# Kernel optimization log

Hardware: AMD Instinct MI355X
Metric: run time of the kernel (lower is better)

The kernel has to match this reference:

```python
import jax, jax.numpy as jnp
import numpy as np

SR = 2  # sr_ratio

def _avgpool2x2(x):
    # x: [B,C,H,W] -> [B,C,H//2,W//2]
    B, C, H, W = x.shape
    return x.reshape(B, C, H // SR, SR, W // SR, SR).mean(axis=(3, 5))

def setup_inputs() -> dict:
    key = jax.random.key(0)
    ks = jax.random.split(key, 6)
    B, C, H, W = 8, 256, 64, 64
    d = C // 8
    sc_qk = 1.0 / np.sqrt(C)
    return {
        "x": jax.random.normal(ks[0], (B, C, H, W), jnp.float32),
        "wq": jax.random.normal(ks[1], (d, C), jnp.float32) * sc_qk,
        "wk": jax.random.normal(ks[2], (d, C), jnp.float32) * sc_qk,
        "wv": jax.random.normal(ks[3], (C, C), jnp.float32) * sc_qk,
        "wo": jax.random.normal(ks[4], (C, C), jnp.float32) * sc_qk,
        "gamma": jax.random.normal(ks[5], (1,), jnp.float32),
    }

def reference(x, wq, wk, wv, wo, gamma):
    B, C, H, W = x.shape
    N = H * W
    d = wq.shape[0]
    # q: conv1x1 then flatten+transpose -> [B, N, d]
    q = jnp.einsum('dc,bchw->bhwd', wq, x).reshape(B, N, d)
    # spatial reduction of K/V source
    x_kv = _avgpool2x2(x)
    Hk, Wk = x_kv.shape[2], x_kv.shape[3]
    Nk = Hk * Wk
    k = jnp.einsum('dc,bchw->bdhw', wk, x_kv).reshape(B, d, Nk)   # [B,d,Nk]
    v = jnp.einsum('oc,bchw->bohw', wv, x_kv).reshape(B, C, Nk)   # [B,C,Nk]
    # attn = softmax(q @ k / sqrt(d)) over Nk
    attn = jax.nn.softmax(jnp.einsum('bnd,bdm->bnm', q, k) / jnp.sqrt(jnp.float32(d)), axis=-1)
    # out = v @ attn^T -> [B,C,N]
    out = jnp.einsum('bcm,bnm->bcn', v, attn).reshape(B, C, H, W)
    out = jnp.einsum('oc,bchw->bohw', wo, out)
    return x + gamma[0] * out
```

## Files before the change

### kernel.cpp

```cpp
#include <hip/hip_runtime.h>

#define BB 8
#define CC 256
#define NN 4096
#define DD 32
#define NK 1024

typedef unsigned short u16;
typedef unsigned int   u32;
typedef __attribute__((ext_vector_type(8))) short bf16x8;
typedef __attribute__((ext_vector_type(4))) float f32x4;

#define MFMA16 __builtin_amdgcn_mfma_f32_16x16x32_bf16

#define OFF_WVO  0u
#define OFF_WQB  32768u
#define OFF_WKB  36864u
#define OFF_QF   40960u
#define OFF_KF   565248u
#define OFF_VOF  696320u

__device__ __forceinline__ u16 f2bf(float f) {
    u32 u = __float_as_uint(f);
    u += 0x7FFFu + ((u >> 16) & 1u);
    return (u16)(u >> 16);
}

__device__ __forceinline__ u32 cvt_pk_bf16(float lo, float hi) {
    u32 r;
    asm("v_cvt_pk_bf16_f32 %0, %1, %2" : "=v"(r) : "v"(lo), "v"(hi));
    return r;
}

__launch_bounds__(1024)
__global__ void wprep_kernel(const float* __restrict__ wq, const float* __restrict__ wk,
                             const float* __restrict__ wv, const float* __restrict__ wo,
                             u16* __restrict__ wqb, u16* __restrict__ wkb,
                             u16* __restrict__ wvob) {
    __shared__ float part[4][256];
    int o = blockIdx.x, t = threadIdx.x;
    int jq = t >> 8, c = t & 255;
    const float* wvp = wv + (size_t)(jq * 64) * CC + c;
    const float* wop = wo + o * CC + jq * 64;
    float acc = 0.f;
#pragma unroll 8
    for (int i = 0; i < 64; ++i)
        acc += wop[i] * wvp[(size_t)i * CC];
    part[jq][c] = acc;
    __syncthreads();
    if (t < 256)
        wvob[o * CC + t] = f2bf(part[0][t] + part[1][t] + part[2][t] + part[3][t]);
    if (o < 8) {
        const float QS = 0.17677669529663687f * 1.4426950408889634f;
        int id = o * 1024 + t;
        wqb[id] = f2bf(wq[id] * QS);
    } else if (o < 16) {
        int id = (o - 8) * 1024 + t;
        wkb[id] = f2bf(wk[id]);
    }
}

__launch_bounds__(256)
__global__ void proj_kernel(const float* __restrict__ x,
                            const u16* __restrict__ wqb, const u16* __restrict__ wkb,
                            const u16* __restrict__ wvob,
                            u16* __restrict__ qF, u16* __restrict__ kF,
                            u16* __restrict__ voF) {
    int t = threadIdx.x, w = t >> 6, l = t & 63, l15 = l & 15, lg = l >> 4;
    const f32x4 fz = {0.f, 0.f, 0.f, 0.f};

    if (blockIdx.x < 256) {
        __shared__ float xl[64 * 136];
        int b = blockIdx.x & 7, nb = blockIdx.x >> 3;
        int n0 = nb * 128;
        f32x4 acc[2][2];
        acc[0][0] = fz; acc[0][1] = fz; acc[1][0] = fz; acc[1][1] = fz;
        int cr = t >> 2, seg = (t & 3) * 32;
        for (int ch = 0; ch < 4; ++ch) {
            int c0 = ch * 64;
            const float* xs = x + ((size_t)(b * CC + c0 + cr)) * NN + n0 + seg;
#pragma unroll
            for (int p = 0; p < 8; ++p)
                *(float4*)&xl[cr * 136 + seg + p * 4] = *(const float4*)(xs + p * 4);
            __syncthreads();
#pragma unroll
            for (int ks = 0; ks < 2; ++ks) {
                int klo = ks * 32 + lg * 8;
#pragma unroll
                for (int i = 0; i < 2; ++i) {
                    int nl = w * 32 + i * 16 + l15;
                    float f0 = xl[(klo + 0) * 136 + nl];
                    float f1 = xl[(klo + 1) * 136 + nl];
                    float f2 = xl[(klo + 2) * 136 + nl];
                    float f3 = xl[(klo + 3) * 136 + nl];
                    float f4 = xl[(klo + 4) * 136 + nl];
                    float f5 = xl[(klo + 5) * 136 + nl];
                    float f6 = xl[(klo + 6) * 136 + nl];
                    float f7 = xl[(klo + 7) * 136 + nl];
                    union { u32 u[4]; bf16x8 v; } cv;
                    cv.u[0] = cvt_pk_bf16(f0, f1);
                    cv.u[1] = cvt_pk_bf16(f2, f3);
                    cv.u[2] = cvt_pk_bf16(f4, f5);
                    cv.u[3] = cvt_pk_bf16(f6, f7);
#pragma unroll
                    for (int dt = 0; dt < 2; ++dt) {
                        bf16x8 bq = *(const bf16x8*)(wqb + (size_t)(dt * 16 + l15) * CC + c0 + klo);
                        acc[i][dt] = MFMA16(cv.v, bq, acc[i][dt], 0, 0, 0);
                    }
                }
            }
            __syncthreads();
        }
        u16* outp = qF + (size_t)b * 256 * 512;
#pragma unroll
        for (int i = 0; i < 2; ++i)
#pragma unroll
            for (int dt = 0; dt < 2; ++dt)
#pragma unroll
                for (int r2 = 0; r2 < 4; ++r2) {
                    int tile = nb * 8 + w * 2 + i;
                    int dhi = dt * 2 + (l15 >> 3);
                    outp[((size_t)tile * 64 + dhi * 16 + lg * 4 + r2) * 8 + (l15 & 7)]
                        = f2bf(acc[i][dt][r2]);
                }
    } else {
        __shared__ u16 pl[64 * 42];
        int blk2 = blockIdx.x - 256;
        int b = blk2 & 7, hk = blk2 >> 3;
        f32x4 acck = fz;
        f32x4 accv[2][4];
#pragma unroll
        for (int mt = 0; mt < 2; ++mt)
#pragma unroll
            for (int ot = 0; ot < 4; ++ot) accv[mt][ot] = fz;

        int cr = t >> 2, w8 = (t & 3) * 8;
        for (int ch = 0; ch < 4; ++ch) {
            int c0 = ch * 64;
            const float* xs = x + ((size_t)(b * CC + c0 + cr)) * NN + (2 * hk) * 64 + w8 * 2;
            float4 A0 = *(const float4*)(xs +  0), A1 = *(const float4*)(xs +  4);
            float4 A2 = *(const float4*)(xs +  8), A3 = *(const float4*)(xs + 12);
            float4 B0 = *(const float4*)(xs + 64), B1 = *(const float4*)(xs + 68);
            float4 B2 = *(const float4*)(xs + 72), B3 = *(const float4*)(xs + 76);
            float p0 = 0.25f * (A0.x + A0.y + B0.x + B0.y);
            float p1 = 0.25f * (A0.z + A0.w + B0.z + B0.w);
            float p2 = 0.25f * (A1.x + A1.y + B1.x + B1.y);
            float p3 = 0.25f * (A1.z + A1.w + B1.z + B1.w);
            float p4 = 0.25f * (A2.x + A2.y + B2.x + B2.y);
            float p5 = 0.25f * (A2.z + A2.w + B2.z + B2.w);
            float p6 = 0.25f * (A3.x + A3.y + B3.x + B3.y);
            float p7 = 0.25f * (A3.z + A3.w + B3.z + B3.w);
            u32* pw = (u32*)&pl[cr * 42 + w8];
            pw[0] = cvt_pk_bf16(p0, p1);
            pw[1] = cvt_pk_bf16(p2, p3);
            pw[2] = cvt_pk_bf16(p4, p5);
            pw[3] = cvt_pk_bf16(p6, p7);
            __syncthreads();
#pragma unroll
            for (int ks = 0; ks < 2; ++ks) {
                int klo = ks * 32 + lg * 8;
                bf16x8 pm[2];
#pragma unroll
                for (int mt = 0; mt < 2; ++mt) {
                    union { u16 s[8]; bf16x8 v; } cv;
#pragma unroll
                    for (int j = 0; j < 8; ++j)
                        cv.s[j] = pl[(klo + j) * 42 + mt * 16 + l15];
                    pm[mt] = cv.v;
                }
                {
                    bf16x8 bk = *(const bf16x8*)(wkb + (size_t)((w & 1) * 16 + l15) * CC + c0 + klo);
                    acck = MFMA16(pm[w >> 1], bk, acck, 0, 0, 0);
                }
#pragma unroll
                for (int ot = 0; ot < 4; ++ot) {
                    bf16x8 ao = *(const bf16x8*)(wvob + (size_t)(w * 64 + ot * 16 + l15) * CC + c0 + klo);
#pragma unroll
                    for (int mt = 0; mt < 2; ++mt)
                        accv[mt][ot] = MFMA16(ao, pm[mt], accv[mt][ot], 0, 0, 0);
                }
            }
            __syncthreads();
        }
#pragma unroll
        for (int r2 = 0; r2 < 4; ++r2)
            kF[((size_t)(b * 64 + hk * 2 + (w >> 1)) * 64
                + ((w & 1) * 2 + (l15 >> 3)) * 16 + lg * 4 + r2) * 8 + (l15 & 7)]
                = f2bf(acck[r2]);
#pragma unroll
        for (int mt = 0; mt < 2; ++mt)
#pragma unroll
            for (int ot = 0; ot < 4; ++ot)
#pragma unroll
                for (int r2 = 0; r2 < 4; ++r2)
                    voF[(((size_t)(b * 32 + hk) * 16 + w * 4 + ot) * 64
                         + (mt * 2 + (l15 >> 3)) * 16 + lg * 4 + r2) * 8 + (l15 & 7)]
                        = f2bf(accv[mt][ot][r2]);
    }
}

__launch_bounds__(512, 4)
__global__ void attn_kernel(const u16* __restrict__ qF, const u16* __restrict__ kF,
                            const u16* __restrict__ voF, const float* __restrict__ x,
                            const float* __restrict__ gamma, float* __restrict__ out) {
    __shared__ __align__(16) u16   p_lds[2][2][64 * 40];
    __shared__ __align__(16) float rs_lds[2][64];

    const int t   = threadIdx.x;
    const int wv  = t >> 6, l = t & 63;
    const int wm  = wv >> 2, wo = wv & 3;
    const int l15 = l & 15, lg = l >> 4;
    const int b   = blockIdx.x & 7;
    const int n0  = (blockIdx.x >> 3) << 6;

    bf16x8 qf = *(const bf16x8*)(qF + ((size_t)(b * 256 + (n0 >> 4) + wo) * 64 + l) * 8);
    const u16* kfp = kF  + ((size_t)(b * 64 + wm * 32) * 64 + l) * 8;
    const u16* vbl = voF + ((size_t)((b * 32 + wm * 16) * 16 + wo * 4) * 64 + l) * 8;

    u16*       pwp = &p_lds[wm][0][(wo * 16 + l15) * 40 + lg * 4];
    const u16* prp = &p_lds[wm][0][l15 * 40 + lg * 8];

    f32x4 acc[4][4];
    const f32x4 fz = {0.f, 0.f, 0.f, 0.f};
#pragma unroll
    for (int j = 0; j < 4; ++j)
#pragma unroll
        for (int of = 0; of < 4; ++of) acc[j][of] = fz;
    float rs = 0.f;

    bf16x8 kf0 = *(const bf16x8*)(kfp);
    bf16x8 kf1 = *(const bf16x8*)(kfp + 512);

#pragma unroll 2
    for (int i = 0; i < 16; ++i) {
        const int buf = i & 1;
        bf16x8 vof[4];
#pragma unroll
        for (int of = 0; of < 4; ++of)
            vof[of] = *(const bf16x8*)(vbl + (size_t)i * 8192 + of * 512);
        f32x4 c0 = MFMA16(kf0, qf, fz, 0, 0, 0);
        f32x4 c1 = MFMA16(kf1, qf, fz, 0, 0, 0);
        float e0 = __builtin_amdgcn_exp2f(c0[0]);
        float e1 = __builtin_amdgcn_exp2f(c0[1]);
        float e2 = __builtin_amdgcn_exp2f(c0[2]);
        float e3 = __builtin_amdgcn_exp2f(c0[3]);
        float e4 = __builtin_amdgcn_exp2f(c1[0]);
        float e5 = __builtin_amdgcn_exp2f(c1[1]);
        float e6 = __builtin_amdgcn_exp2f(c1[2]);
        float e7 = __builtin_amdgcn_exp2f(c1[3]);
        rs += (e0 + e1 + e2 + e3) + (e4 + e5 + e6 + e7);
        uint2 pw0, pw1;
        pw0.x = cvt_pk_bf16(e0, e1);
        pw0.y = cvt_pk_bf16(e2, e3);
        pw1.x = cvt_pk_bf16(e4, e5);
        pw1.y = cvt_pk_bf16(e6, e7);
        u16* pw = pwp + buf * 2560;
        *(uint2*)pw        = pw0;
        *(uint2*)(pw + 16) = pw1;
        asm volatile("s_waitcnt lgkmcnt(0)" ::: "memory");
        __builtin_amdgcn_s_barrier();
        bf16x8 kn0, kn1;
        if (i < 15) {
            kn0 = *(const bf16x8*)(kfp + (size_t)(i * 2 + 2) * 512);
            kn1 = *(const bf16x8*)(kfp + (size_t)(i * 2 + 3) * 512);
        }
        const u16* pr = prp + buf * 2560;
        __builtin_amdgcn_s_setprio(1);
#pragma unroll
        for (int j = 0; j < 4; ++j) {
            bf16x8 pa = *(const bf16x8*)(pr + j * 640);
#pragma unroll
            for (int of = 0; of < 4; ++of)
                acc[j][of] = MFMA16(pa, vof[of], acc[j][of], 0, 0, 0);
        }
        __builtin_amdgcn_s_setprio(0);
        kf0 = kn0; kf1 = kn1;
    }

    rs += __shfl_xor(rs, 16);
    rs += __shfl_xor(rs, 32);
    if (l < 16) rs_lds[wm][wo * 16 + l] = rs;

    __syncthreads();
    float* cbuf = (float*)p_lds;
#pragma unroll
    for (int r = 0; r < 4; ++r) {
        if (wm == 1) {
#pragma unroll
            for (int of = 0; of < 4; ++of)
                *(float4*)&cbuf[((wo * 64 + l) * 16) + of * 4] =
                    make_float4(acc[r][of][0], acc[r][of][1], acc[r][of][2], acc[r][of][3]);
        }
        __syncthreads();
        if (wm == 0) {
#pragma unroll
            for (int of = 0; of < 4; ++of) {
                float4 p = *(const float4*)&cbuf[((wo * 64 + l) * 16) + of * 4];
                acc[r][of][0] += p.x; acc[r][of][1] += p.y;
                acc[r][of][2] += p.z; acc[r][of][3] += p.w;
            }
        }
        __syncthreads();
    }

    if (wm == 0) {
        float g = gamma[0];
#pragma unroll
        for (int j = 0; j < 4; ++j) {
            float r0 = rs_lds[0][j * 16 + lg * 4 + 0] + rs_lds[1][j * 16 + lg * 4 + 0];
            float r1 = rs_lds[0][j * 16 + lg * 4 + 1] + rs_lds[1][j * 16 + lg * 4 + 1];
            float r2 = rs_lds[0][j * 16 + lg * 4 + 2] + rs_lds[1][j * 16 + lg * 4 + 2];
            float r3 = rs_lds[0][j * 16 + lg * 4 + 3] + rs_lds[1][j * 16 + lg * 4 + 3];
            float fa0 = g / r0, fa1 = g / r1, fa2 = g / r2, fa3 = g / r3;
#pragma unroll
            for (int of = 0; of < 4; ++of) {
                size_t base = ((size_t)(b * CC + wo * 64 + of * 16 + l15)) * NN
                            + n0 + j * 16 + lg * 4;
                float4 xv = *(const float4*)(x + base);
                float4 ov;
                ov.x = xv.x + acc[j][of][0] * fa0;
                ov.y = xv.y + acc[j][of][1] * fa1;
                ov.z = xv.z + acc[j][of][2] * fa2;
                ov.w = xv.w + acc[j][of][3] * fa3;
                *(float4*)(out + base) = ov;
            }
        }
    }
}

extern "C" void kernel_launch(void* const* d_in, const int* in_sizes, int n_in,
                              void* d_out, int out_size, void* d_ws, size_t ws_size,
                              hipStream_t stream) {
    const float* x     = (const float*)d_in[0];
    const float* wq    = (const float*)d_in[1];
    const float* wk    = (const float*)d_in[2];
    const float* wv    = (const float*)d_in[3];
    const float* wo    = (const float*)d_in[4];
    const float* gamma = (const float*)d_in[5];
    float* out = (float*)d_out;
    float* ws  = (float*)d_ws;

    u16* wvob = (u16*)(ws + OFF_WVO);
    u16* wqb  = (u16*)(ws + OFF_WQB);
    u16* wkb  = (u16*)(ws + OFF_WKB);
    u16* qF   = (u16*)(ws + OFF_QF);
    u16* kF   = (u16*)(ws + OFF_KF);
    u16* voF  = (u16*)(ws + OFF_VOF);

    wprep_kernel<<<dim3(256), dim3(1024), 0, stream>>>(wq, wk, wv, wo, wqb, wkb, wvob);
    proj_kernel <<<dim3(512), dim3(256),  0, stream>>>(x, wqb, wkb, wvob, qF, kF, voF);
    attn_kernel <<<dim3(512), dim3(512),  0, stream>>>(qF, kF, voF, x, gamma, out);
}
```

Baseline: 59.59 us.

## Fuse Q and KV projection blocks and restructure attention split over query rows

The projection kernel now has each block load an x tile once and produce both the Q projection and the pooled K/V projections from the same shared-memory tile. It also prefetches the next channel chunk into registers. This halves the x global reads and the grid size. The attention kernel now splits waves over query rows instead of over the key dimension, which removes the cross-wave LDS reduction of accumulators. It also software-pipelines the QK exp step one iteration ahead of the PV MFMAs. In exchange there are fewer blocks (256), lower occupancy (launch bounds 2), and a longer serial loop per wave.

```diff
diff --git a/kernel.cpp b/kernel.cpp
--- a/kernel.cpp
+++ b/kernel.cpp
@@ -66,51 +66,108 @@
                             const u16* __restrict__ wvob,
                             u16* __restrict__ qF, u16* __restrict__ kF,
                             u16* __restrict__ voF) {
+    __shared__ float xl[64 * 136];
+    __shared__ u16 pl[64 * 42];
     int t = threadIdx.x, w = t >> 6, l = t & 63, l15 = l & 15, lg = l >> 4;
     const f32x4 fz = {0.f, 0.f, 0.f, 0.f};
-
-    if (blockIdx.x < 256) {
-        __shared__ float xl[64 * 136];
-        int b = blockIdx.x & 7, nb = blockIdx.x >> 3;
-        int n0 = nb * 128;
-        f32x4 acc[2][2];
-        acc[0][0] = fz; acc[0][1] = fz; acc[1][0] = fz; acc[1][1] = fz;
-        int cr = t >> 2, seg = (t & 3) * 32;
-        for (int ch = 0; ch < 4; ++ch) {
-            int c0 = ch * 64;
-            const float* xs = x + ((size_t)(b * CC + c0 + cr)) * NN + n0 + seg;
-#pragma unroll
-            for (int p = 0; p < 8; ++p)
-                *(float4*)&xl[cr * 136 + seg + p * 4] = *(const float4*)(xs + p * 4);
-            __syncthreads();
-#pragma unroll
-            for (int ks = 0; ks < 2; ++ks) {
-                int klo = ks * 32 + lg * 8;
-#pragma unroll
-                for (int i = 0; i < 2; ++i) {
-                    int nl = w * 32 + i * 16 + l15;
-                    float f0 = xl[(klo + 0) * 136 + nl];
-                    float f1 = xl[(klo + 1) * 136 + nl];
-                    float f2 = xl[(klo + 2) * 136 + nl];
-                    float f3 = xl[(klo + 3) * 136 + nl];
-                    float f4 = xl[(klo + 4) * 136 + nl];
-                    float f5 = xl[(klo + 5) * 136 + nl];
-                    float f6 = xl[(klo + 6) * 136 + nl];
-                    float f7 = xl[(klo + 7) * 136 + nl];
-                    union { u32 u[4]; bf16x8 v; } cv;
-                    cv.u[0] = cvt_pk_bf16(f0, f1);
-                    cv.u[1] = cvt_pk_bf16(f2, f3);
-                    cv.u[2] = cvt_pk_bf16(f4, f5);
-                    cv.u[3] = cvt_pk_bf16(f6, f7);
-#pragma unroll
-                    for (int dt = 0; dt < 2; ++dt) {
-                        bf16x8 bq = *(const bf16x8*)(wqb + (size_t)(dt * 16 + l15) * CC + c0 + klo);
-                        acc[i][dt] = MFMA16(cv.v, bq, acc[i][dt], 0, 0, 0);
-                    }
+    int b = blockIdx.x & 7, hb = blockIdx.x >> 3;
+    int n0 = hb * 128;
+
+    int cr = t >> 2, seg = (t & 3) * 32, w8 = (t & 3) * 8;
+
+    f32x4 qacc[2][2];
+    qacc[0][0] = fz; qacc[0][1] = fz; qacc[1][0] = fz; qacc[1][1] = fz;
+    f32x4 kacc = fz;
+    f32x4 vacc[2][4];
+#pragma unroll
+    for (int mt = 0; mt < 2; ++mt)
+#pragma unroll
+        for (int ot = 0; ot < 4; ++ot) vacc[mt][ot] = fz;
+
+    float4 xreg[8];
+    {
+        const float* xs = x + ((size_t)(b * CC + cr)) * NN + n0 + seg;
+#pragma unroll
+        for (int p = 0; p < 8; ++p) xreg[p] = *(const float4*)(xs + p * 4);
+    }
+
+    for (int ch = 0; ch < 4; ++ch) {
+        int c0 = ch * 64;
+#pragma unroll
+        for (int p = 0; p < 8; ++p)
+            *(float4*)&xl[cr * 136 + seg + p * 4] = xreg[p];
+        __syncthreads();
+        if (ch < 3) {
+            const float* xs = x + ((size_t)(b * CC + c0 + 64 + cr)) * NN + n0 + seg;
+#pragma unroll
+            for (int p = 0; p < 8; ++p) xreg[p] = *(const float4*)(xs + p * 4);
+        }
+        {
+            const float* xr = &xl[cr * 136];
+            u32 pw[4];
+#pragma unroll
+            for (int j = 0; j < 4; ++j) {
+                int q0 = 2 * (w8 + 2 * j), q1 = 2 * (w8 + 2 * j + 1);
+                float v0 = 0.25f * (xr[q0] + xr[q0 + 1] + xr[64 + q0] + xr[65 + q0]);
+                float v1 = 0.25f * (xr[q1] + xr[q1 + 1] + xr[64 + q1] + xr[65 + q1]);
+                pw[j] = cvt_pk_bf16(v0, v1);
+            }
+            u32* pd = (u32*)&pl[cr * 42 + w8];
+            pd[0] = pw[0]; pd[1] = pw[1]; pd[2] = pw[2]; pd[3] = pw[3];
+        }
+#pragma unroll
+        for (int ks = 0; ks < 2; ++ks) {
+            int klo = ks * 32 + lg * 8;
+#pragma unroll
+            for (int i = 0; i < 2; ++i) {
+                int nl = w * 32 + i * 16 + l15;
+                float f0 = xl[(klo + 0) * 136 + nl];
+                float f1 = xl[(klo + 1) * 136 + nl];
+                float f2 = xl[(klo + 2) * 136 + nl];
+                float f3 = xl[(klo + 3) * 136 + nl];
+                float f4 = xl[(klo + 4) * 136 + nl];
+                float f5 = xl[(klo + 5) * 136 + nl];
+                float f6 = xl[(klo + 6) * 136 + nl];
+                float f7 = xl[(klo + 7) * 136 + nl];
+                union { u32 u[4]; bf16x8 v; } cv;
+                cv.u[0] = cvt_pk_bf16(f0, f1);
+                cv.u[1] = cvt_pk_bf16(f2, f3);
+                cv.u[2] = cvt_pk_bf16(f4, f5);
+                cv.u[3] = cvt_pk_bf16(f6, f7);
+#pragma unroll
+                for (int dt = 0; dt < 2; ++dt) {
+                    bf16x8 bq = *(const bf16x8*)(wqb + (size_t)(dt * 16 + l15) * CC + c0 + klo);
+                    qacc[i][dt] = MFMA16(cv.v, bq, qacc[i][dt], 0, 0, 0);
                 }
             }
-            __syncthreads();
-        }
+        }
+        __syncthreads();
+#pragma unroll
+        for (int ks = 0; ks < 2; ++ks) {
+            int klo = ks * 32 + lg * 8;
+            bf16x8 pm[2];
+#pragma unroll
+            for (int mt = 0; mt < 2; ++mt) {
+                union { u16 s[8]; bf16x8 v; } cv;
+#pragma unroll
+                for (int j = 0; j < 8; ++j)
+                    cv.s[j] = pl[(klo + j) * 42 + mt * 16 + l15];
+                pm[mt] = cv.v;
+            }
+            {
+                bf16x8 bk = *(const bf16x8*)(wkb + (size_t)((w & 1) * 16 + l15) * CC + c0 + klo);
+                kacc = MFMA16(pm[w >> 1], bk, kacc, 0, 0, 0);
+            }
+#pragma unroll
+            for (int ot = 0; ot < 4; ++ot) {
+                bf16x8 ao = *(const bf16x8*)(wvob + (size_t)(w * 64 + ot * 16 + l15) * CC + c0 + klo);
+#pragma unroll
+                for (int mt = 0; mt < 2; ++mt)
+                    vacc[mt][ot] = MFMA16(ao, pm[mt], vacc[mt][ot], 0, 0, 0);
+            }
+        }
+    }
+    {
         u16* outp = qF + (size_t)b * 256 * 512;
 #pragma unroll
         for (int i = 0; i < 2; ++i)
@@ -118,107 +175,48 @@
             for (int dt = 0; dt < 2; ++dt)
 #pragma unroll
                 for (int r2 = 0; r2 < 4; ++r2) {
-                    int tile = nb * 8 + w * 2 + i;
+                    int tile = hb * 8 + w * 2 + i;
                     int dhi = dt * 2 + (l15 >> 3);
                     outp[((size_t)tile * 64 + dhi * 16 + lg * 4 + r2) * 8 + (l15 & 7)]
-                        = f2bf(acc[i][dt][r2]);
+                        = f2bf(qacc[i][dt][r2]);
                 }
-    } else {
-        __shared__ u16 pl[64 * 42];
-        int blk2 = blockIdx.x - 256;
-        int b = blk2 & 7, hk = blk2 >> 3;
-        f32x4 acck = fz;
-        f32x4 accv[2][4];
-#pragma unroll
-        for (int mt = 0; mt < 2; ++mt)
-#pragma unroll
-            for (int ot = 0; ot < 4; ++ot) accv[mt][ot] = fz;
-
-        int cr = t >> 2, w8 = (t & 3) * 8;
-        for (int ch = 0; ch < 4; ++ch) {
-            int c0 = ch * 64;
-            const float* xs = x + ((size_t)(b * CC + c0 + cr)) * NN + (2 * hk) * 64 + w8 * 2;
-            float4 A0 = *(const float4*)(xs +  0), A1 = *(const float4*)(xs +  4);
-            float4 A2 = *(const float4*)(xs +  8), A3 = *(const float4*)(xs + 12);
-            float4 B0 = *(const float4*)(xs + 64), B1 = *(const float4*)(xs + 68);
-            float4 B2 = *(const float4*)(xs + 72), B3 = *(const float4*)(xs + 76);
-            float p0 = 0.25f * (A0.x + A0.y + B0.x + B0.y);
-            float p1 = 0.25f * (A0.z + A0.w + B0.z + B0.w);
-            float p2 = 0.25f * (A1.x + A1.y + B1.x + B1.y);
-            float p3 = 0.25f * (A1.z + A1.w + B1.z + B1.w);
-            float p4 = 0.25f * (A2.x + A2.y + B2.x + B2.y);
-            float p5 = 0.25f * (A2.z + A2.w + B2.z + B2.w);
-            float p6 = 0.25f * (A3.x + A3.y + B3.x + B3.y);
-            float p7 = 0.25f * (A3.z + A3.w + B3.z + B3.w);
-            u32* pw = (u32*)&pl[cr * 42 + w8];
-            pw[0] = cvt_pk_bf16(p0, p1);
-            pw[1] = cvt_pk_bf16(p2, p3);
-            pw[2] = cvt_pk_bf16(p4, p5);
-            pw[3] = cvt_pk_bf16(p6, p7);
-            __syncthreads();
-#pragma unroll
-            for (int ks = 0; ks < 2; ++ks) {
-                int klo = ks * 32 + lg * 8;
-                bf16x8 pm[2];
-#pragma unroll
-                for (int mt = 0; mt < 2; ++mt) {
-                    union { u16 s[8]; bf16x8 v; } cv;
-#pragma unroll
-                    for (int j = 0; j < 8; ++j)
-                        cv.s[j] = pl[(klo + j) * 42 + mt * 16 + l15];
-                    pm[mt] = cv.v;
-                }
-                {
-                    bf16x8 bk = *(const bf16x8*)(wkb + (size_t)((w & 1) * 16 + l15) * CC + c0 + klo);
-                    acck = MFMA16(pm[w >> 1], bk, acck, 0, 0, 0);
-                }
-#pragma unroll
-                for (int ot = 0; ot < 4; ++ot) {
-                    bf16x8 ao = *(const bf16x8*)(wvob + (size_t)(w * 64 + ot * 16 + l15) * CC + c0 + klo);
-#pragma unroll
-                    for (int mt = 0; mt < 2; ++mt)
-                        accv[mt][ot] = MFMA16(ao, pm[mt], accv[mt][ot], 0, 0, 0);
-                }
-            }
-            __syncthreads();
-        }
-#pragma unroll
-        for (int r2 = 0; r2 < 4; ++r2)
-            kF[((size_t)(b * 64 + hk * 2 + (w >> 1)) * 64
-                + ((w & 1) * 2 + (l15 >> 3)) * 16 + lg * 4 + r2) * 8 + (l15 & 7)]
-                = f2bf(acck[r2]);
-#pragma unroll
-        for (int mt = 0; mt < 2; ++mt)
-#pragma unroll
-            for (int ot = 0; ot < 4; ++ot)
-#pragma unroll
-                for (int r2 = 0; r2 < 4; ++r2)
-                    voF[(((size_t)(b * 32 + hk) * 16 + w * 4 + ot) * 64
-                         + (mt * 2 + (l15 >> 3)) * 16 + lg * 4 + r2) * 8 + (l15 & 7)]
-                        = f2bf(accv[mt][ot][r2]);
-    }
-}
-
-__launch_bounds__(512, 4)
+    }
+#pragma unroll
+    for (int r2 = 0; r2 < 4; ++r2)
+        kF[((size_t)(b * 64 + hb * 2 + (w >> 1)) * 64
+            + ((w & 1) * 2 + (l15 >> 3)) * 16 + lg * 4 + r2) * 8 + (l15 & 7)]
+            = f2bf(kacc[r2]);
+#pragma unroll
+    for (int mt = 0; mt < 2; ++mt)
+#pragma unroll
+        for (int ot = 0; ot < 4; ++ot)
+#pragma unroll
+            for (int r2 = 0; r2 < 4; ++r2)
+                voF[(((size_t)(b * 32 + hb) * 16 + w * 4 + ot) * 64
+                     + (mt * 2 + (l15 >> 3)) * 16 + lg * 4 + r2) * 8 + (l15 & 7)]
+                    = f2bf(vacc[mt][ot][r2]);
+}
+
+__launch_bounds__(512, 2)
 __global__ void attn_kernel(const u16* __restrict__ qF, const u16* __restrict__ kF,
                             const u16* __restrict__ voF, const float* __restrict__ x,
                             const float* __restrict__ gamma, float* __restrict__ out) {
     __shared__ __align__(16) u16   p_lds[2][2][64 * 40];
-    __shared__ __align__(16) float rs_lds[2][64];
+    __shared__ __align__(16) float rs_lds[128];
 
     const int t   = threadIdx.x;
     const int wv  = t >> 6, l = t & 63;
-    const int wm  = wv >> 2, wo = wv & 3;
+    const int nh  = wv >> 2, wo4 = wv & 3;
     const int l15 = l & 15, lg = l >> 4;
     const int b   = blockIdx.x & 7;
-    const int n0  = (blockIdx.x >> 3) << 6;
-
-    bf16x8 qf = *(const bf16x8*)(qF + ((size_t)(b * 256 + (n0 >> 4) + wo) * 64 + l) * 8);
-    const u16* kfp = kF  + ((size_t)(b * 64 + wm * 32) * 64 + l) * 8;
-    const u16* vbl = voF + ((size_t)((b * 32 + wm * 16) * 16 + wo * 4) * 64 + l) * 8;
-
-    u16*       pwp = &p_lds[wm][0][(wo * 16 + l15) * 40 + lg * 4];
-    const u16* prp = &p_lds[wm][0][l15 * 40 + lg * 8];
+    const int n0  = (blockIdx.x >> 3) << 7;
+
+    bf16x8 qf = *(const bf16x8*)(qF + ((size_t)(b * 256 + (n0 >> 4) + nh * 4 + wo4) * 64 + l) * 8);
+    const u16* kfp = kF  + ((size_t)(b * 64) * 64 + l) * 8;
+    const u16* vbl = voF + ((size_t)((b * 32) * 16 + wo4 * 4) * 64 + l) * 8;
+
+    u16*       pwp = &p_lds[nh][0][(wo4 * 16 + l15) * 40 + lg * 4];
+    const u16* prp = &p_lds[nh][0][l15 * 40 + lg * 8];
 
     f32x4 acc[4][4];
     const f32x4 fz = {0.f, 0.f, 0.f, 0.f};
@@ -230,14 +228,7 @@
 
     bf16x8 kf0 = *(const bf16x8*)(kfp);
     bf16x8 kf1 = *(const bf16x8*)(kfp + 512);
-
-#pragma unroll 2
-    for (int i = 0; i < 16; ++i) {
-        const int buf = i & 1;
-        bf16x8 vof[4];
-#pragma unroll
-        for (int of = 0; of < 4; ++of)
-            vof[of] = *(const bf16x8*)(vbl + (size_t)i * 8192 + of * 512);
+    {
         f32x4 c0 = MFMA16(kf0, qf, fz, 0, 0, 0);
         f32x4 c1 = MFMA16(kf1, qf, fz, 0, 0, 0);
         float e0 = __builtin_amdgcn_exp2f(c0[0]);
@@ -254,76 +245,86 @@
         pw0.y = cvt_pk_bf16(e2, e3);
         pw1.x = cvt_pk_bf16(e4, e5);
         pw1.y = cvt_pk_bf16(e6, e7);
-        u16* pw = pwp + buf * 2560;
-        *(uint2*)pw        = pw0;
-        *(uint2*)(pw + 16) = pw1;
+        *(uint2*)pwp        = pw0;
+        *(uint2*)(pwp + 16) = pw1;
+    }
+    kf0 = *(const bf16x8*)(kfp + 2 * 512);
+    kf1 = *(const bf16x8*)(kfp + 3 * 512);
+    asm volatile("s_waitcnt lgkmcnt(0)" ::: "memory");
+    __builtin_amdgcn_s_barrier();
+
+#pragma unroll 2
+    for (int i = 0; i < 32; ++i) {
+        const int buf = i & 1;
+        bf16x8 vof[4];
+#pragma unroll
+        for (int of = 0; of < 4; ++of)
+            vof[of] = *(const bf16x8*)(vbl + (size_t)i * 8192 + of * 512);
+        bf16x8 kn0, kn1;
+        if (i < 31) {
+            f32x4 c0 = MFMA16(kf0, qf, fz, 0, 0, 0);
+            f32x4 c1 = MFMA16(kf1, qf, fz, 0, 0, 0);
+            if (i < 30) {
+                kn0 = *(const bf16x8*)(kfp + (size_t)(2 * i + 4) * 512);
+                kn1 = *(const bf16x8*)(kfp + (size_t)(2 * i + 5) * 512);
+            }
+            float e0 = __builtin_amdgcn_exp2f(c0[0]);
+            float e1 = __builtin_amdgcn_exp2f(c0[1]);
+            float e2 = __builtin_amdgcn_exp2f(c0[2]);
+            float e3 = __builtin_amdgcn_exp2f(c0[3]);
+            float e4 = __builtin_amdgcn_exp2f(c1[0]);
+            float e5 = __builtin_amdgcn_exp2f(c1[1]);
+            float e6 = __builtin_amdgcn_exp2f(c1[2]);
+            float e7 = __builtin_amdgcn_exp2f(c1[3]);
+            rs += (e0 + e1 + e2 + e3) + (e4 + e5 + e6 + e7);
+            uint2 pw0, pw1;
+            pw0.x = cvt_pk_bf16(e0, e1);
+            pw0.y = cvt_pk_bf16(e2, e3);
+            pw1.x = cvt_pk_bf16(e4, e5);
+            pw1.y = cvt_pk_bf16(e6, e7);
+            u16* pw = pwp + (buf ^ 1) * 2560;
+            *(uint2*)pw        = pw0;
+            *(uint2*)(pw + 16) = pw1;
+        }
+        const u16* pr = prp + buf * 2560;
+        __builtin_amdgcn_s_setprio(1);
+#pragma unroll
+        for (int j = 0; j < 4; ++j) {
+            bf16x8 pa = *(const bf16x8*)(pr + j * 640);
+#pragma unroll
+            for (int of = 0; of < 4; ++of)
+                acc[j][of] = MFMA16(pa, vof[of], acc[j][of], 0, 0, 0);
+        }
+        __builtin_amdgcn_s_setprio(0);
         asm volatile("s_waitcnt lgkmcnt(0)" ::: "memory");
         __builtin_amdgcn_s_barrier();
-        bf16x8 kn0, kn1;
-        if (i < 15) {
-            kn0 = *(const bf16x8*)(kfp + (size_t)(i * 2 + 2) * 512);
-            kn1 = *(const bf16x8*)(kfp + (size_t)(i * 2 + 3) * 512);
-        }
-        const u16* pr = prp + buf * 2560;
-        __builtin_amdgcn_s_setprio(1);
-#pragma unroll
-        for (int j = 0; j < 4; ++j) {
-            bf16x8 pa = *(const bf16x8*)(pr + j * 640);
-#pragma unroll
-            for (int of = 0; of < 4; ++of)
-                acc[j][of] = MFMA16(pa, vof[of], acc[j][of], 0, 0, 0);
-        }
-        __builtin_amdgcn_s_setprio(0);
         kf0 = kn0; kf1 = kn1;
     }
 
     rs += __shfl_xor(rs, 16);
     rs += __shfl_xor(rs, 32);
-    if (l < 16) rs_lds[wm][wo * 16 + l] = rs;
-
+    if (l < 16) rs_lds[nh * 64 + wo4 * 16 + l] = rs;
     __syncthreads();
-    float* cbuf = (float*)p_lds;
-#pragma unroll
-    for (int r = 0; r < 4; ++r) {
-        if (wm == 1) {
-#pragma unroll
-            for (int of = 0; of < 4; ++of)
-                *(float4*)&cbuf[((wo * 64 + l) * 16) + of * 4] =
-                    make_float4(acc[r][of][0], acc[r][of][1], acc[r][of][2], acc[r][of][3]);
-        }
-        __syncthreads();
-        if (wm == 0) {
-#pragma unroll
-            for (int of = 0; of < 4; ++of) {
-                float4 p = *(const float4*)&cbuf[((wo * 64 + l) * 16) + of * 4];
-                acc[r][of][0] += p.x; acc[r][of][1] += p.y;
-                acc[r][of][2] += p.z; acc[r][of][3] += p.w;
-            }
-        }
-        __syncthreads();
-    }
-
-    if (wm == 0) {
-        float g = gamma[0];
-#pragma unroll
-        for (int j = 0; j < 4; ++j) {
-            float r0 = rs_lds[0][j * 16 + lg * 4 + 0] + rs_lds[1][j * 16 + lg * 4 + 0];
-            float r1 = rs_lds[0][j * 16 + lg * 4 + 1] + rs_lds[1][j * 16 + lg * 4 + 1];
-            float r2 = rs_lds[0][j * 16 + lg * 4 + 2] + rs_lds[1][j * 16 + lg * 4 + 2];
-            float r3 = rs_lds[0][j * 16 + lg * 4 + 3] + rs_lds[1][j * 16 + lg * 4 + 3];
-            float fa0 = g / r0, fa1 = g / r1, fa2 = g / r2, fa3 = g / r3;
-#pragma unroll
-            for (int of = 0; of < 4; ++of) {
-                size_t base = ((size_t)(b * CC + wo * 64 + of * 16 + l15)) * NN
-                            + n0 + j * 16 + lg * 4;
-                float4 xv = *(const float4*)(x + base);
-                float4 ov;
-                ov.x = xv.x + acc[j][of][0] * fa0;
-                ov.y = xv.y + acc[j][of][1] * fa1;
-                ov.z = xv.z + acc[j][of][2] * fa2;
-                ov.w = xv.w + acc[j][of][3] * fa3;
-                *(float4*)(out + base) = ov;
-            }
+
+    float g = gamma[0];
+#pragma unroll
+    for (int j = 0; j < 4; ++j) {
+        int rbase = nh * 64 + j * 16 + lg * 4;
+        float fa0 = g / rs_lds[rbase + 0];
+        float fa1 = g / rs_lds[rbase + 1];
+        float fa2 = g / rs_lds[rbase + 2];
+        float fa3 = g / rs_lds[rbase + 3];
+#pragma unroll
+        for (int of = 0; of < 4; ++of) {
+            size_t base = ((size_t)(b * CC + wo4 * 64 + of * 16 + l15)) * NN
+                        + n0 + nh * 64 + j * 16 + lg * 4;
+            float4 xv = *(const float4*)(x + base);
+            float4 ov;
+            ov.x = xv.x + acc[j][of][0] * fa0;
+            ov.y = xv.y + acc[j][of][1] * fa1;
+            ov.z = xv.z + acc[j][of][2] * fa2;
+            ov.w = xv.w + acc[j][of][3] * fa3;
+            *(float4*)(out + base) = ov;
         }
     }
 }
@@ -348,6 +349,6 @@
     u16* voF  = (u16*)(ws + OFF_VOF);
 
     wprep_kernel<<<dim3(256), dim3(1024), 0, stream>>>(wq, wk, wv, wo, wqb, wkb, wvob);
-    proj_kernel <<<dim3(512), dim3(256),  0, stream>>>(x, wqb, wkb, wvob, qF, kF, voF);
-    attn_kernel <<<dim3(512), dim3(512),  0, stream>>>(qF, kF, voF, x, gamma, out);
-}
+    proj_kernel <<<dim3(256), dim3(256),  0, stream>>>(x, wqb, wkb, wvob, qF, kF, voF);
+    attn_kernel <<<dim3(256), dim3(512),  0, stream>>>(qF, kF, voF, x, gamma, out);
+}
```

New measurement: 71.93 us. 20.7% more time.

## Software-pipeline QK^T/exp stage one tile ahead of PV MFMAs

Applied to the files above, without the earlier changes.

Peels the first score tile (QK MFMA, exp2, bf16 pack, LDS store) into a prologue. Inside the loop it computes the next tile's probabilities into the other LDS buffer while doing the PV MFMAs on the current buffer. The result is one barrier per iteration placed after both stages, so exp/MFMA latency of the next tile overlaps the current accumulation. This costs extra register pressure and more complex control flow at the loop tail.

```diff
diff --git a/kernel.cpp b/kernel.cpp
--- a/kernel.cpp
+++ b/kernel.cpp
@@ -230,14 +230,7 @@
 
     bf16x8 kf0 = *(const bf16x8*)(kfp);
     bf16x8 kf1 = *(const bf16x8*)(kfp + 512);
-
-#pragma unroll 2
-    for (int i = 0; i < 16; ++i) {
-        const int buf = i & 1;
-        bf16x8 vof[4];
-#pragma unroll
-        for (int of = 0; of < 4; ++of)
-            vof[of] = *(const bf16x8*)(vbl + (size_t)i * 8192 + of * 512);
+    {
         f32x4 c0 = MFMA16(kf0, qf, fz, 0, 0, 0);
         f32x4 c1 = MFMA16(kf1, qf, fz, 0, 0, 0);
         float e0 = __builtin_amdgcn_exp2f(c0[0]);
@@ -254,26 +247,59 @@
         pw0.y = cvt_pk_bf16(e2, e3);
         pw1.x = cvt_pk_bf16(e4, e5);
         pw1.y = cvt_pk_bf16(e6, e7);
-        u16* pw = pwp + buf * 2560;
-        *(uint2*)pw        = pw0;
-        *(uint2*)(pw + 16) = pw1;
+        *(uint2*)pwp        = pw0;
+        *(uint2*)(pwp + 16) = pw1;
+    }
+    kf0 = *(const bf16x8*)(kfp + 2 * 512);
+    kf1 = *(const bf16x8*)(kfp + 3 * 512);
+    asm volatile("s_waitcnt lgkmcnt(0)" ::: "memory");
+    __builtin_amdgcn_s_barrier();
+
+#pragma unroll 2
+    for (int i = 0; i < 16; ++i) {
+        const int buf = i & 1;
+        bf16x8 vof[4];
+#pragma unroll
+        for (int of = 0; of < 4; ++of)
+            vof[of] = *(const bf16x8*)(vbl + (size_t)i * 8192 + of * 512);
+        bf16x8 kn0, kn1;
+        if (i < 15) {
+            f32x4 c0 = MFMA16(kf0, qf, fz, 0, 0, 0);
+            f32x4 c1 = MFMA16(kf1, qf, fz, 0, 0, 0);
+            if (i < 14) {
+                kn0 = *(const bf16x8*)(kfp + (size_t)(2 * i + 4) * 512);
+                kn1 = *(const bf16x8*)(kfp + (size_t)(2 * i + 5) * 512);
+            }
+            float e0 = __builtin_amdgcn_exp2f(c0[0]);
+            float e1 = __builtin_amdgcn_exp2f(c0[1]);
+            float e2 = __builtin_amdgcn_exp2f(c0[2]);
+            float e3 = __builtin_amdgcn_exp2f(c0[3]);
+            float e4 = __builtin_amdgcn_exp2f(c1[0]);
+            float e5 = __builtin_amdgcn_exp2f(c1[1]);
+            float e6 = __builtin_amdgcn_exp2f(c1[2]);
+            float e7 = __builtin_amdgcn_exp2f(c1[3]);
+            rs += (e0 + e1 + e2 + e3) + (e4 + e5 + e6 + e7);
+            uint2 pw0, pw1;
+            pw0.x = cvt_pk_bf16(e0, e1);
+            pw0.y = cvt_pk_bf16(e2, e3);
+            pw1.x = cvt_pk_bf16(e4, e5);
+            pw1.y = cvt_pk_bf16(e6, e7);
+            u16* pw = pwp + (buf ^ 1) * 2560;
+            *(uint2*)pw        = pw0;
+            *(uint2*)(pw + 16) = pw1;
+        }
+        const u16* pr = prp + buf * 2560;
+        __builtin_amdgcn_s_setprio(1);
+#pragma unroll
+        for (int j = 0; j < 4; ++j) {
+            bf16x8 pa = *(const bf16x8*)(pr + j * 640);
+#pragma unroll
+            for (int of = 0; of < 4; ++of)
+                acc[j][of] = MFMA16(pa, vof[of], acc[j][of], 0, 0, 0);
+        }
+        __builtin_amdgcn_s_setprio(0);
         asm volatile("s_waitcnt lgkmcnt(0)" ::: "memory");
         __builtin_amdgcn_s_barrier();
-        bf16x8 kn0, kn1;
-        if (i < 15) {
-            kn0 = *(const bf16x8*)(kfp + (size_t)(i * 2 + 2) * 512);
-            kn1 = *(const bf16x8*)(kfp + (size_t)(i * 2 + 3) * 512);
-        }
-        const u16* pr = prp + buf * 2560;
-        __builtin_amdgcn_s_setprio(1);
-#pragma unroll
-        for (int j = 0; j < 4; ++j) {
-            bf16x8 pa = *(const bf16x8*)(pr + j * 640);
-#pragma unroll
-            for (int of = 0; of < 4; ++of)
-                acc[j][of] = MFMA16(pa, vof[of], acc[j][of], 0, 0, 0);
-        }
-        __builtin_amdgcn_s_setprio(0);
         kf0 = kn0; kf1 = kn1;
     }
 
```

Result: no change. 59.88 us (+0.5%).

## Switch attention kernel to 32x32 MFMA with register-shuffled probabilities

Applied to the files above, without the earlier changes.

Rewrites the attention kernel to use 32x32x16 bf16 MFMA tiles, so each wave computes a full 32-query score block and feeds the exponentiated probabilities straight back as the A operand via cross-half lane shuffles instead of staging them through LDS with barriers. Work is split by query chunk and output-channel half, and each wave loops over all 1024 keys, which removes the cross-wave LDS reduction of partial outputs. The proj kernel's Q/K/VO output layouts are changed to match the 32x32 fragment format. The trade-off is fewer threads per block, more accumulator registers per wave, and each wave re-reading K and VO for the whole key range.

```diff
diff --git a/kernel.cpp b/kernel.cpp
--- a/kernel.cpp
+++ b/kernel.cpp
@@ -8,10 +8,12 @@
 
 typedef unsigned short u16;
 typedef unsigned int   u32;
-typedef __attribute__((ext_vector_type(8))) short bf16x8;
-typedef __attribute__((ext_vector_type(4))) float f32x4;
+typedef __attribute__((ext_vector_type(8)))  short bf16x8;
+typedef __attribute__((ext_vector_type(4)))  float f32x4;
+typedef __attribute__((ext_vector_type(16))) float f32x16;
 
 #define MFMA16 __builtin_amdgcn_mfma_f32_16x16x32_bf16
+#define MFMA32 __builtin_amdgcn_mfma_f32_32x32x16_bf16
 
 #define OFF_WVO  0u
 #define OFF_WQB  32768u
@@ -111,17 +113,16 @@
             }
             __syncthreads();
         }
-        u16* outp = qF + (size_t)b * 256 * 512;
+        u16* outp = qF + (size_t)b * 131072;
 #pragma unroll
         for (int i = 0; i < 2; ++i)
 #pragma unroll
             for (int dt = 0; dt < 2; ++dt)
 #pragma unroll
                 for (int r2 = 0; r2 < 4; ++r2) {
-                    int tile = nb * 8 + w * 2 + i;
-                    int dhi = dt * 2 + (l15 >> 3);
-                    outp[((size_t)tile * 64 + dhi * 16 + lg * 4 + r2) * 8 + (l15 & 7)]
-                        = f2bf(acc[i][dt][r2]);
+                    int n = nb * 128 + w * 32 + i * 16 + lg * 4 + r2;
+                    outp[(((size_t)(n >> 5) * 2 + dt) * 64 + (n & 31) + 32 * (l15 >> 3)) * 8
+                         + (l15 & 7)] = f2bf(acc[i][dt][r2]);
                 }
     } else {
         __shared__ u16 pl[64 * 42];
@@ -183,147 +184,123 @@
             __syncthreads();
         }
 #pragma unroll
-        for (int r2 = 0; r2 < 4; ++r2)
-            kF[((size_t)(b * 64 + hk * 2 + (w >> 1)) * 64
-                + ((w & 1) * 2 + (l15 >> 3)) * 16 + lg * 4 + r2) * 8 + (l15 & 7)]
+        for (int r2 = 0; r2 < 4; ++r2) {
+            int m31 = (w >> 1) * 16 + lg * 4 + r2;
+            kF[(size_t)b * 32768
+               + (((size_t)hk * 2 + (w & 1)) * 64 + m31 + 32 * (l15 >> 3)) * 8 + (l15 & 7)]
                 = f2bf(acck[r2]);
+        }
 #pragma unroll
         for (int mt = 0; mt < 2; ++mt)
 #pragma unroll
             for (int ot = 0; ot < 4; ++ot)
 #pragma unroll
-                for (int r2 = 0; r2 < 4; ++r2)
-                    voF[(((size_t)(b * 32 + hk) * 16 + w * 4 + ot) * 64
-                         + (mt * 2 + (l15 >> 3)) * 16 + lg * 4 + r2) * 8 + (l15 & 7)]
-                        = f2bf(accv[mt][ot][r2]);
+                for (int r2 = 0; r2 < 4; ++r2) {
+                    int o  = w * 64 + ot * 16 + lg * 4 + r2;
+                    int m16c = hk * 2 + mt;
+                    voF[(size_t)b * 262144
+                        + (((size_t)m16c * 8 + (o >> 5)) * 64 + (o & 31) + 32 * (l15 >> 3)) * 8
+                        + (l15 & 7)] = f2bf(accv[mt][ot][r2]);
+                }
     }
 }
 
-__launch_bounds__(512, 4)
+__launch_bounds__(256, 2)
 __global__ void attn_kernel(const u16* __restrict__ qF, const u16* __restrict__ kF,
                             const u16* __restrict__ voF, const float* __restrict__ x,
                             const float* __restrict__ gamma, float* __restrict__ out) {
-    __shared__ __align__(16) u16   p_lds[2][2][64 * 40];
-    __shared__ __align__(16) float rs_lds[2][64];
+    __shared__ float rs_lds[4][32];
 
     const int t   = threadIdx.x;
-    const int wv  = t >> 6, l = t & 63;
-    const int wm  = wv >> 2, wo = wv & 3;
-    const int l15 = l & 15, lg = l >> 4;
+    const int w   = t >> 6, l = t & 63;
+    const int l31 = l & 31, hi = l >> 5;
     const int b   = blockIdx.x & 7;
-    const int n0  = (blockIdx.x >> 3) << 6;
-
-    bf16x8 qf = *(const bf16x8*)(qF + ((size_t)(b * 256 + (n0 >> 4) + wo) * 64 + l) * 8);
-    const u16* kfp = kF  + ((size_t)(b * 64 + wm * 32) * 64 + l) * 8;
-    const u16* vbl = voF + ((size_t)((b * 32 + wm * 16) * 16 + wo * 4) * 64 + l) * 8;
-
-    u16*       pwp = &p_lds[wm][0][(wo * 16 + l15) * 40 + lg * 4];
-    const u16* prp = &p_lds[wm][0][l15 * 40 + lg * 8];
-
-    f32x4 acc[4][4];
-    const f32x4 fz = {0.f, 0.f, 0.f, 0.f};
-#pragma unroll
-    for (int j = 0; j < 4; ++j)
-#pragma unroll
-        for (int of = 0; of < 4; ++of) acc[j][of] = fz;
+    const int rem = blockIdx.x >> 3;
+    const int oh  = rem & 1;
+    const int nc  = (rem >> 1) * 4 + w;
+
+    const u16* qb = qF  + (size_t)b * 131072;
+    const u16* kb = kF  + (size_t)b * 32768;
+    const u16* vb = voF + (size_t)b * 262144;
+
+    bf16x8 qf0 = *(const bf16x8*)(qb + ((size_t)(nc * 2 + 0) * 64 + l) * 8);
+    bf16x8 qf1 = *(const bf16x8*)(qb + ((size_t)(nc * 2 + 1) * 64 + l) * 8);
+
+    f32x16 acc[4];
+    f32x16 fz16;
+#pragma unroll
+    for (int i = 0; i < 16; ++i) fz16[i] = 0.f;
+#pragma unroll
+    for (int c = 0; c < 4; ++c) acc[c] = fz16;
     float rs = 0.f;
 
-    bf16x8 kf0 = *(const bf16x8*)(kfp);
-    bf16x8 kf1 = *(const bf16x8*)(kfp + 512);
-
-#pragma unroll 2
-    for (int i = 0; i < 16; ++i) {
-        const int buf = i & 1;
-        bf16x8 vof[4];
-#pragma unroll
-        for (int of = 0; of < 4; ++of)
-            vof[of] = *(const bf16x8*)(vbl + (size_t)i * 8192 + of * 512);
-        f32x4 c0 = MFMA16(kf0, qf, fz, 0, 0, 0);
-        f32x4 c1 = MFMA16(kf1, qf, fz, 0, 0, 0);
-        float e0 = __builtin_amdgcn_exp2f(c0[0]);
-        float e1 = __builtin_amdgcn_exp2f(c0[1]);
-        float e2 = __builtin_amdgcn_exp2f(c0[2]);
-        float e3 = __builtin_amdgcn_exp2f(c0[3]);
-        float e4 = __builtin_amdgcn_exp2f(c1[0]);
-        float e5 = __builtin_amdgcn_exp2f(c1[1]);
-        float e6 = __builtin_amdgcn_exp2f(c1[2]);
-        float e7 = __builtin_amdgcn_exp2f(c1[3]);
-        rs += (e0 + e1 + e2 + e3) + (e4 + e5 + e6 + e7);
-        uint2 pw0, pw1;
-        pw0.x = cvt_pk_bf16(e0, e1);
-        pw0.y = cvt_pk_bf16(e2, e3);
-        pw1.x = cvt_pk_bf16(e4, e5);
-        pw1.y = cvt_pk_bf16(e6, e7);
-        u16* pw = pwp + buf * 2560;
-        *(uint2*)pw        = pw0;
-        *(uint2*)(pw + 16) = pw1;
-        asm volatile("s_waitcnt lgkmcnt(0)" ::: "memory");
-        __builtin_amdgcn_s_barrier();
+    bf16x8 kf0 = *(const bf16x8*)(kb + ((size_t)0 * 64 + l) * 8);
+    bf16x8 kf1 = *(const bf16x8*)(kb + ((size_t)1 * 64 + l) * 8);
+
+#pragma unroll 1
+    for (int mc = 0; mc < 32; ++mc) {
+        bf16x8 vo[2][4];
+#pragma unroll
+        for (int mt = 0; mt < 2; ++mt)
+#pragma unroll
+            for (int c = 0; c < 4; ++c)
+                vo[mt][c] = *(const bf16x8*)(vb +
+                    (((size_t)(2 * mc + mt) * 8 + oh * 4 + c) * 64 + l) * 8);
+        f32x16 ss = MFMA32(kf0, qf0, fz16, 0, 0, 0);
+        ss = MFMA32(kf1, qf1, ss, 0, 0, 0);
         bf16x8 kn0, kn1;
-        if (i < 15) {
-            kn0 = *(const bf16x8*)(kfp + (size_t)(i * 2 + 2) * 512);
-            kn1 = *(const bf16x8*)(kfp + (size_t)(i * 2 + 3) * 512);
-        }
-        const u16* pr = prp + buf * 2560;
-        __builtin_amdgcn_s_setprio(1);
-#pragma unroll
-        for (int j = 0; j < 4; ++j) {
-            bf16x8 pa = *(const bf16x8*)(pr + j * 640);
-#pragma unroll
-            for (int of = 0; of < 4; ++of)
-                acc[j][of] = MFMA16(pa, vof[of], acc[j][of], 0, 0, 0);
-        }
-        __builtin_amdgcn_s_setprio(0);
+        if (mc < 31) {
+            kn0 = *(const bf16x8*)(kb + ((size_t)((mc + 1) * 2 + 0) * 64 + l) * 8);
+            kn1 = *(const bf16x8*)(kb + ((size_t)((mc + 1) * 2 + 1) * 64 + l) * 8);
+        }
+        float e[16];
+#pragma unroll
+        for (int r = 0; r < 16; ++r) {
+            e[r] = __builtin_amdgcn_exp2f(ss[r]);
+            rs += e[r];
+        }
+        u32 X  = cvt_pk_bf16(e[0],  e[1]),  Z  = cvt_pk_bf16(e[2],  e[3]);
+        u32 Y  = cvt_pk_bf16(e[4],  e[5]),  W  = cvt_pk_bf16(e[6],  e[7]);
+        u32 X2 = cvt_pk_bf16(e[8],  e[9]),  Z2 = cvt_pk_bf16(e[10], e[11]);
+        u32 Y2 = cvt_pk_bf16(e[12], e[13]), W2 = cvt_pk_bf16(e[14], e[15]);
+        u32 Xp  = __shfl_xor(X, 32),  Zp  = __shfl_xor(Z, 32);
+        u32 Yp  = __shfl_xor(Y, 32),  Wp  = __shfl_xor(W, 32);
+        u32 X2p = __shfl_xor(X2, 32), Z2p = __shfl_xor(Z2, 32);
+        u32 Y2p = __shfl_xor(Y2, 32), W2p = __shfl_xor(W2, 32);
+        bool lo = (hi == 0);
+        union { u32 u[4]; bf16x8 v; } paA, paB;
+        paA.u[0] = lo ? X  : Yp;   paA.u[1] = lo ? Z  : Wp;
+        paA.u[2] = lo ? Xp : Y;    paA.u[3] = lo ? Zp : W;
+        paB.u[0] = lo ? X2  : Y2p; paB.u[1] = lo ? Z2  : W2p;
+        paB.u[2] = lo ? X2p : Y2;  paB.u[3] = lo ? Z2p : W2;
+#pragma unroll
+        for (int c = 0; c < 4; ++c) {
+            acc[c] = MFMA32(paA.v, vo[0][c], acc[c], 0, 0, 0);
+            acc[c] = MFMA32(paB.v, vo[1][c], acc[c], 0, 0, 0);
+        }
         kf0 = kn0; kf1 = kn1;
     }
 
-    rs += __shfl_xor(rs, 16);
     rs += __shfl_xor(rs, 32);
-    if (l < 16) rs_lds[wm][wo * 16 + l] = rs;
-
-    __syncthreads();
-    float* cbuf = (float*)p_lds;
-#pragma unroll
-    for (int r = 0; r < 4; ++r) {
-        if (wm == 1) {
-#pragma unroll
-            for (int of = 0; of < 4; ++of)
-                *(float4*)&cbuf[((wo * 64 + l) * 16) + of * 4] =
-                    make_float4(acc[r][of][0], acc[r][of][1], acc[r][of][2], acc[r][of][3]);
-        }
-        __syncthreads();
-        if (wm == 0) {
-#pragma unroll
-            for (int of = 0; of < 4; ++of) {
-                float4 p = *(const float4*)&cbuf[((wo * 64 + l) * 16) + of * 4];
-                acc[r][of][0] += p.x; acc[r][of][1] += p.y;
-                acc[r][of][2] += p.z; acc[r][of][3] += p.w;
-            }
-        }
-        __syncthreads();
-    }
-
-    if (wm == 0) {
-        float g = gamma[0];
-#pragma unroll
-        for (int j = 0; j < 4; ++j) {
-            float r0 = rs_lds[0][j * 16 + lg * 4 + 0] + rs_lds[1][j * 16 + lg * 4 + 0];
-            float r1 = rs_lds[0][j * 16 + lg * 4 + 1] + rs_lds[1][j * 16 + lg * 4 + 1];
-            float r2 = rs_lds[0][j * 16 + lg * 4 + 2] + rs_lds[1][j * 16 + lg * 4 + 2];
-            float r3 = rs_lds[0][j * 16 + lg * 4 + 3] + rs_lds[1][j * 16 + lg * 4 + 3];
-            float fa0 = g / r0, fa1 = g / r1, fa2 = g / r2, fa3 = g / r3;
-#pragma unroll
-            for (int of = 0; of < 4; ++of) {
-                size_t base = ((size_t)(b * CC + wo * 64 + of * 16 + l15)) * NN
-                            + n0 + j * 16 + lg * 4;
-                float4 xv = *(const float4*)(x + base);
-                float4 ov;
-                ov.x = xv.x + acc[j][of][0] * fa0;
-                ov.y = xv.y + acc[j][of][1] * fa1;
-                ov.z = xv.z + acc[j][of][2] * fa2;
-                ov.w = xv.w + acc[j][of][3] * fa3;
-                *(float4*)(out + base) = ov;
-            }
+    if (l < 32) rs_lds[w][l] = rs;
+
+    float g = gamma[0];
+#pragma unroll
+    for (int q = 0; q < 4; ++q) {
+        float4 R = *(const float4*)&rs_lds[w][4 * hi + 8 * q];
+        float fa0 = g / R.x, fa1 = g / R.y, fa2 = g / R.z, fa3 = g / R.w;
+#pragma unroll
+        for (int c = 0; c < 4; ++c) {
+            int o = oh * 128 + c * 32 + l31;
+            int n = nc * 32 + 8 * q + 4 * hi;
+            size_t base = ((size_t)(b * CC + o)) * NN + n;
+            float4 xv = *(const float4*)(x + base);
+            float4 ov;
+            ov.x = xv.x + acc[c][4 * q + 0] * fa0;
+            ov.y = xv.y + acc[c][4 * q + 1] * fa1;
+            ov.z = xv.z + acc[c][4 * q + 2] * fa2;
+            ov.w = xv.w + acc[c][4 * q + 3] * fa3;
+            *(float4*)(out + base) = ov;
         }
     }
 }
@@ -349,5 +326,5 @@
 
     wprep_kernel<<<dim3(256), dim3(1024), 0, stream>>>(wq, wk, wv, wo, wqb, wkb, wvob);
     proj_kernel <<<dim3(512), dim3(256),  0, stream>>>(x, wqb, wkb, wvob, qF, kF, voF);
-    attn_kernel <<<dim3(512), dim3(512),  0, stream>>>(qF, kF, voF, x, gamma, out);
-}
+    attn_kernel <<<dim3(512), dim3(256),  0, stream>>>(qF, kF, voF, x, gamma, out);
+}
```

New measurement: 66.03 us. 10.8% more time.
